# Kernel optimization log

Hardware: AMD Instinct MI355X
Metric: run time of the kernel (lower is better)

The kernel has to match this reference:

```python
import jax, jax.numpy as jnp
import numpy as np

N_NODES = 50000
N_EDGES = 800000
IN_C, HID_C, OUT_C = 256, 128, 64


def setup_inputs() -> dict:
    key = jax.random.key(0)
    k1, k2, k3, k4 = jax.random.split(key, 4)
    x = jax.random.normal(k1, (N_NODES, IN_C), dtype=jnp.float32)
    edge_index = jax.random.randint(k2, (2, N_EDGES), 0, N_NODES, dtype=jnp.int64)
    # Glorot-ish init for GCNConv weights; zero bias (PyG default)
    W1 = jax.random.normal(k3, (IN_C, HID_C), dtype=jnp.float32) * (1.0 / np.sqrt(IN_C))
    b1 = jnp.zeros((HID_C,), dtype=jnp.float32)
    W2 = jax.random.normal(k4, (HID_C, OUT_C), dtype=jnp.float32) * (1.0 / np.sqrt(HID_C))
    b2 = jnpform = jnp.zeros((OUT_C,), dtype=jnp.float32)
    return {"x": x, "edge_index": edge_index, "W1": W1, "b1": b1, "W2": W2, "b2": b2}


def _gcn_conv(x, src, dst, W, b, n_nodes):
    """PyG GCNConv: out = D^-1/2 (A+I) D^-1/2 x W + b (self-loops already in src/dst)."""
    h = x @ W  # [N, out] dense GEMM first (in >= out)
    deg = jax.ops.segment_sum(jnp.ones_like(dst, dtype=h.dtype), dst,
                              num_segments=n_nodes)  # includes self-loops -> deg >= 1
    dinv = jax.lax.rsqrt(jnp.maximum(deg, 1.0))
    norm = dinv[src] * dinv[dst]  # [E+N]
    msg = h[src] * norm[:, None]  # gather + scale
    out = jax.ops.segment_sum(msg, dst, num_segments=n_nodes)  # scatter-add
    return out + b


def reference(x, edge_index, W1, b1, W2, b2):
    n = x.shape[0]
    loops = jnp.arange(n, dtype=edge_index.dtype)
    src = jnp.concatenate([edge_index[0], loops])
    dst = jnp.concatenate([edge_index[1], loops])
    h = jax.nn.relu(_gcn_conv(x, src, dst, W1, b1, n))
    return _gcn_conv(h, src, dst, W2, b2, n)
```

## Files before the change

### kernel.cpp

```cpp
#include <hip/hip_runtime.h>

#define N_NODES 50000
#define N_EDGES 800000
#define IN_C    256
#define HID_C   128
#define OUT_C   64

#define SCAN_CHUNK 512
#define SCAN_NB ((N_NODES + SCAN_CHUNK - 1) / SCAN_CHUNK)

#define NBK 391
#define PCH 2048
#define NPB ((N_EDGES + PCH - 1) / PCH)

typedef __attribute__((ext_vector_type(8))) __bf16 bf16x8;
typedef __attribute__((ext_vector_type(4))) float f32x4;

__device__ __forceinline__ unsigned short f2bf(float f) {
    union { float f; unsigned int u; } c{f};
    unsigned int r = c.u + 0x7FFFu + ((c.u >> 16) & 1u);
    return (unsigned short)(r >> 16);
}
__device__ __forceinline__ float bf2f(unsigned short b) {
    union { unsigned int u; float f; } c{(unsigned int)b << 16};
    return c.f;
}

__global__ void deg_kernel(const int* __restrict__ src,
                           const int* __restrict__ dst,
                           unsigned int* __restrict__ deg, int E,
                           const float* __restrict__ W1,
                           const float* __restrict__ W2,
                           unsigned short* __restrict__ Wt1,
                           unsigned short* __restrict__ Wt2) {
    const int bid = blockIdx.x;
    const int t   = threadIdx.x;
    if (Wt1 != nullptr && bid < 40) {
        if (bid < 32) {
            int e = bid * 1024 + t * 4;
            float4 v = *(const float4*)&W1[e];
            int k = e >> 7, c = e & 127;
            Wt1[(c + 0) * IN_C + k] = f2bf(v.x);
            Wt1[(c + 1) * IN_C + k] = f2bf(v.y);
            Wt1[(c + 2) * IN_C + k] = f2bf(v.z);
            Wt1[(c + 3) * IN_C + k] = f2bf(v.w);
        } else {
            int e = (bid - 32) * 1024 + t * 4;
            float4 v = *(const float4*)&W2[e];
            int k = e >> 6, c = e & 63;
            Wt2[(c + 0) * HID_C + k] = f2bf(v.x);
            Wt2[(c + 1) * HID_C + k] = f2bf(v.y);
            Wt2[(c + 2) * HID_C + k] = f2bf(v.z);
            Wt2[(c + 3) * HID_C + k] = f2bf(v.w);
        }
    }
    int i = bid * blockDim.x + t;
    if (i < E) {
        int s = src[i];
        int d = dst[i];
        if ((unsigned)s < N_NODES && (unsigned)d < N_NODES)
            atomicAdd(&deg[d], 1u);
    }
}

__global__ __launch_bounds__(256) void scan1_kernel(
        unsigned int* __restrict__ cur, unsigned int* __restrict__ bsum,
        float* __restrict__ dinv, int N) {
    __shared__ unsigned int lds[256];
    const int b = blockIdx.x;
    const int t = threadIdx.x;
    const int i0 = b * SCAN_CHUNK + 2 * t;

    unsigned e0 = (i0     < N) ? cur[i0]     : 0u;
    unsigned e1 = (i0 + 1 < N) ? cur[i0 + 1] : 0u;
    if (i0     < N) dinv[i0]     = rsqrtf((float)(e0 + 1u));
    if (i0 + 1 < N) dinv[i0 + 1] = rsqrtf((float)(e1 + 1u));

    unsigned p = e0 + e1;
    lds[t] = p;
    __syncthreads();
    for (int off = 1; off < 256; off <<= 1) {
        unsigned v = (t >= off) ? lds[t - off] : 0u;
        __syncthreads();
        lds[t] += v;
        __syncthreads();
    }
    unsigned excl = lds[t] - p;
    if (t == 255) bsum[b] = lds[255];
    if (i0     < N) cur[i0]     = excl;
    if (i0 + 1 < N) cur[i0 + 1] = excl + e0;
}

__global__ __launch_bounds__(256) void scan2_kernel(
        unsigned int* __restrict__ cur, const unsigned int* __restrict__ bsum,
        int N) {
    __shared__ unsigned int lds[256];
    const int b = blockIdx.x;
    const int t = threadIdx.x;
    lds[t] = (t < b && t < SCAN_NB) ? bsum[t] : 0u;
    __syncthreads();
    for (int off = 128; off > 0; off >>= 1) {
        if (t < off) lds[t] += lds[t + off];
        __syncthreads();
    }
    const unsigned offset = lds[0];
    const int i0 = b * SCAN_CHUNK + 2 * t;
    if (i0     < N) cur[i0]     += offset;
    if (i0 + 1 < N) cur[i0 + 1] += offset;
}

__global__ void binit_kernel(const unsigned int* __restrict__ cur,
                             unsigned int* __restrict__ bcur,
                             unsigned int* __restrict__ bbase) {
    int t = threadIdx.x;
    if (t < NBK) {
        unsigned v = cur[t * 128];
        bcur[t]  = v;
        bbase[t] = v;
    }
    if (t == NBK) bbase[NBK] = N_EDGES;
}

template <int KDIM, int NDIM>
__global__ __launch_bounds__(256) void fused_gemm_part_kernel(
        const float* __restrict__ A, const unsigned short* __restrict__ Wt,
        const float* __restrict__ dinv,
        unsigned short* __restrict__ Cout, int M,
        const int* __restrict__ src, const int* __restrict__ dst,
        unsigned int* __restrict__ bcur,
        unsigned int* __restrict__ gpairs, int E) {
    __shared__ union {
        struct { unsigned short A[64][40]; unsigned short B[NDIM][40]; } g;
        struct { unsigned int pairs[PCH];
                 unsigned int counts[512];
                 unsigned int starts[513];
                 unsigned int gbase[NBK];
                 unsigned int temp[256]; } p;
    } sh;

    const int bid  = blockIdx.x;
    const int t    = threadIdx.x;
    const int role = bid % 3;
    const int pb   = bid / 3;

    if (role == 2) {
        const int base = pb * PCH;
        for (int i = t; i < 512; i += 256) sh.p.counts[i] = 0;
        __syncthreads();

        unsigned preg[PCH / 256], rreg[PCH / 256];
        bool val[PCH / 256];
#pragma unroll
        for (int j = 0; j < PCH / 256; ++j) {
            int i = base + j * 256 + t;
            val[j] = false;
            if (i < E) {
                int s = src[i], d = dst[i];
                if ((unsigned)s < N_NODES && (unsigned)d < N_NODES) {
                    val[j] = true;
                    unsigned bkt = (unsigned)d >> 7;
                    preg[j] = (bkt << 23) | (((unsigned)d & 127u) << 16) |
                              (unsigned)s;
                    rreg[j] = atomicAdd(&sh.p.counts[bkt], 1u);
                }
            }
        }
        __syncthreads();
        unsigned e0 = sh.p.counts[2 * t], e1 = sh.p.counts[2 * t + 1];
        unsigned pp = e0 + e1;
        sh.p.temp[t] = pp;
        __syncthreads();
        for (int off = 1; off < 256; off <<= 1) {
            unsigned v = (t >= off) ? sh.p.temp[t - off] : 0u;
            __syncthreads();
            sh.p.temp[t] += v;
            __syncthreads();
        }
        unsigned excl = sh.p.temp[t] - pp;
        sh.p.starts[2 * t]     = excl;
        sh.p.starts[2 * t + 1] = excl + e0;
        if (t == 255) sh.p.starts[512] = sh.p.temp[255];
        __syncthreads();
        for (int b = t; b < NBK; b += 256) {
            unsigned c = sh.p.counts[b];
            if (c) sh.p.gbase[b] = atomicAdd(&bcur[b], c);
        }
        __syncthreads();
#pragma unroll
        for (int j = 0; j < PCH / 256; ++j)
            if (val[j]) {
                unsigned bkt  = preg[j] >> 23;
                unsigned slot = sh.p.starts[bkt] + rreg[j];
                sh.p.pairs[slot] = preg[j];
            }
        __syncthreads();
        unsigned total = sh.p.starts[512];
        for (unsigned i = t; i < total; i += 256) {
            unsigned pd  = sh.p.pairs[i];
            unsigned bkt = pd >> 23;
            unsigned rank = i - sh.p.starts[bkt];
            gpairs[sh.p.gbase[bkt] + rank] = pd;
        }
        return;
    }

    const int gb = pb * 2 + role;
    if (gb >= (M + 63) / 64) return;
    constexpr int NF = NDIM / 16;
    const int block_row = gb * 64;
    const int w    = t >> 6;
    const int lane = t & 63;
    const int arow = lane & 15;
    const int g    = lane >> 4;

    f32x4 acc[NF] = {};

    for (int k0 = 0; k0 < KDIM; k0 += 32) {
#pragma unroll
        for (int q = 0; q < 2; ++q) {
            int u   = t * 2 + q;
            int row = u >> 3;
            int kq  = u & 7;
            int grow = block_row + row;
            if (grow >= M) grow = M - 1;
            float4 v = *(const float4*)&A[(size_t)grow * KDIM + k0 + kq * 4];
            ushort4 bb = {f2bf(v.x), f2bf(v.y), f2bf(v.z), f2bf(v.w)};
            *(ushort4*)&sh.g.A[row][kq * 4] = bb;
        }
        {
            constexpr int B8 = (NDIM * 4) / 256;
#pragma unroll
            for (int r = 0; r < B8; ++r) {
                int iu  = t * B8 + r;
                int col = iu >> 2;
                int k8  = iu & 3;
                *(uint4*)&sh.g.B[col][k8 * 8] =
                    *(const uint4*)&Wt[(size_t)col * KDIM + k0 + k8 * 8];
            }
        }
        __syncthreads();

        bf16x8 af = *(const bf16x8*)&sh.g.A[w * 16 + arow][g * 8];
#pragma unroll
        for (int f = 0; f < NF; ++f) {
            bf16x8 bf_ = *(const bf16x8*)&sh.g.B[f * 16 + arow][g * 8];
            acc[f] = __builtin_amdgcn_mfma_f32_16x16x32_bf16(af, bf_, acc[f],
                                                             0, 0, 0);
        }
        __syncthreads();
    }

#pragma unroll
    for (int i = 0; i < 4; ++i) {
        int row = block_row + w * 16 + g * 4 + i;
        if (row < M) {
            float dv = dinv[row];
#pragma unroll
            for (int f = 0; f < NF; ++f)
                Cout[(size_t)row * NDIM + f * 16 + arow] = f2bf(dv * acc[f][i]);
        }
    }
}

__global__ __launch_bounds__(256) void fine_fill_kernel(
        const unsigned int* __restrict__ gpairs,
        const unsigned int* __restrict__ bbase,
        unsigned int* __restrict__ cur,
        int* __restrict__ esrc, int N) {
    __shared__ unsigned int cnt[128];
    __shared__ unsigned int inc[128];
    const int b  = blockIdx.x;
    const int t  = threadIdx.x;
    const unsigned e0 = bbase[b], e1 = bbase[b + 1];
    const int node0 = b << 7;
    const int nn = min(128, N - node0);

    if (t < 128) cnt[t] = 0;
    __syncthreads();
    for (unsigned i = e0 + t; i < e1; i += 256) {
        unsigned dloc = (gpairs[i] >> 16) & 127u;
        atomicAdd(&cnt[dloc], 1u);
    }
    __syncthreads();
    if (t < 128) inc[t] = cnt[t];
    __syncthreads();
    for (int off = 1; off < 128; off <<= 1) {
        unsigned a = (t >= off && t < 128) ? inc[t - off] : 0u;
        __syncthreads();
        if (t < 128) inc[t] += a;
        __syncthreads();
    }
    if (t < 128) cnt[t] = inc[t] - cnt[t];
    __syncthreads();
    for (unsigned i = e0 + t; i < e1; i += 256) {
        unsigned pd   = gpairs[i];
        unsigned dloc = (pd >> 16) & 127u;
        unsigned r = atomicAdd(&cnt[dloc], 1u);
        esrc[e0 + r] = (int)(pd & 0xFFFFu);
    }
    __syncthreads();
    if (t < nn) cur[node0 + t] = e0 + inc[t];
}

template <int KDIM, int NDIM, bool ABF16>
__global__ __launch_bounds__(256) void mfma_gemm_kernel(
        const void* __restrict__ Ain, const unsigned short* __restrict__ Wt,
        const float* __restrict__ dinv,
        unsigned short* __restrict__ Cout, int M) {
    __shared__ unsigned short Alds[64][40];
    __shared__ unsigned short Blds[NDIM][40];

    const int t = threadIdx.x;
    constexpr int NF = NDIM / 16;
    const int block_row = blockIdx.x * 64;
    const int w    = t >> 6;
    const int lane = t & 63;
    const int arow = lane & 15;
    const int g    = lane >> 4;

    f32x4 acc[NF] = {};

    for (int k0 = 0; k0 < KDIM; k0 += 32) {
        if (ABF16) {
            const unsigned short* A = (const unsigned short*)Ain;
            int row = t >> 2;
            int k8  = t & 3;
            int grow = block_row + row;
            if (grow >= M) grow = M - 1;
            *(uint4*)&Alds[row][k8 * 8] =
                *(const uint4*)&A[(size_t)grow * KDIM + k0 + k8 * 8];
        } else {
            const float* A = (const float*)Ain;
#pragma unroll
            for (int q = 0; q < 2; ++q) {
                int u   = t * 2 + q;
                int row = u >> 3;
                int kq  = u & 7;
                int grow = block_row + row;
                if (grow >= M) grow = M - 1;
                float4 v = *(const float4*)&A[(size_t)grow * KDIM + k0 + kq * 4];
                ushort4 bb = {f2bf(v.x), f2bf(v.y), f2bf(v.z), f2bf(v.w)};
                *(ushort4*)&Alds[row][kq * 4] = bb;
            }
        }
        {
            constexpr int B8 = (NDIM * 4) / 256;
#pragma unroll
            for (int r = 0; r < B8; ++r) {
                int iu  = t * B8 + r;
                int col = iu >> 2;
                int k8  = iu & 3;
                *(uint4*)&Blds[col][k8 * 8] =
                    *(const uint4*)&Wt[(size_t)col * KDIM + k0 + k8 * 8];
            }
        }
        __syncthreads();

        bf16x8 af = *(const bf16x8*)&Alds[w * 16 + arow][g * 8];
#pragma unroll
        for (int f = 0; f < NF; ++f) {
            bf16x8 bf_ = *(const bf16x8*)&Blds[f * 16 + arow][g * 8];
            acc[f] = __builtin_amdgcn_mfma_f32_16x16x32_bf16(af, bf_, acc[f],
                                                             0, 0, 0);
        }
        __syncthreads();
    }

#pragma unroll
    for (int i = 0; i < 4; ++i) {
        int row = block_row + w * 16 + g * 4 + i;
        if (row < M) {
            float dv = dinv[row];
#pragma unroll
            for (int f = 0; f < NF; ++f)
                Cout[(size_t)row * NDIM + f * 16 + arow] = f2bf(dv * acc[f][i]);
        }
    }
}

template <int C, bool RELU, bool OUTBF16>
__global__ __launch_bounds__(256) void gather_kernel(
        const unsigned int* __restrict__ cur,
        const int* __restrict__ esrc,
        const float* __restrict__ dinv,
        const unsigned short* __restrict__ h,
        const float* __restrict__ bias,
        void* __restrict__ out, int N) {
    constexpr int G = C / 4;
    int tid  = blockIdx.x * blockDim.x + threadIdx.x;
    int v    = tid / G;
    int lane = tid % G;
    if (v >= N) return;
    unsigned int start = (v == 0) ? 0u : cur[v - 1];
    unsigned int end   = cur[v];

    ushort4 hs = *(const ushort4*)&h[(size_t)v * C + lane * 4];
    float4 a0 = {bf2f(hs.x), bf2f(hs.y), bf2f(hs.z), bf2f(hs.w)};
    float4 a1 = {0.f, 0.f, 0.f, 0.f};
    float4 a2 = {0.f, 0.f, 0.f, 0.f};
    float4 a3 = {0.f, 0.f, 0.f, 0.f};

    unsigned int e = start;
    for (; e + 4 <= end; e += 4) {
        int s0 = esrc[e + 0];
        int s1 = esrc[e + 1];
        int s2 = esrc[e + 2];
        int s3 = esrc[e + 3];
        ushort4 v0 = *(const ushort4*)&h[(size_t)s0 * C + lane * 4];
        ushort4 v1 = *(const ushort4*)&h[(size_t)s1 * C + lane * 4];
        ushort4 v2 = *(const ushort4*)&h[(size_t)s2 * C + lane * 4];
        ushort4 v3 = *(const ushort4*)&h[(size_t)s3 * C + lane * 4];
        a0.x += bf2f(v0.x); a0.y += bf2f(v0.y); a0.z += bf2f(v0.z); a0.w += bf2f(v0.w);
        a1.x += bf2f(v1.x); a1.y += bf2f(v1.y); a1.z += bf2f(v1.z); a1.w += bf2f(v1.w);
        a2.x += bf2f(v2.x); a2.y += bf2f(v2.y); a2.z += bf2f(v2.z); a2.w += bf2f(v2.w);
        a3.x += bf2f(v3.x); a3.y += bf2f(v3.y); a3.z += bf2f(v3.z); a3.w += bf2f(v3.w);
    }
    for (; e < end; ++e) {
        int s = esrc[e];
        ushort4 v0 = *(const ushort4*)&h[(size_t)s * C + lane * 4];
        a0.x += bf2f(v0.x); a0.y += bf2f(v0.y); a0.z += bf2f(v0.z); a0.w += bf2f(v0.w);
    }
    float4 acc;
    acc.x = (a0.x + a1.x) + (a2.x + a3.x);
    acc.y = (a0.y + a1.y) + (a2.y + a3.y);
    acc.z = (a0.z + a1.z) + (a2.z + a3.z);
    acc.w = (a0.w + a1.w) + (a2.w + a3.w);

    float dv = dinv[v];
    float4 b = *(const float4*)&bias[lane * 4];
    float4 r;
    r.x = fmaf(dv, acc.x, b.x);
    r.y = fmaf(dv, acc.y, b.y);
    r.z = fmaf(dv, acc.z, b.z);
    r.w = fmaf(dv, acc.w, b.w);
    if (RELU) {
        r.x = fmaxf(r.x, 0.f);
        r.y = fmaxf(r.y, 0.f);
        r.z = fmaxf(r.z, 0.f);
        r.w = fmaxf(r.w, 0.f);
    }
    if (OUTBF16) {
        ushort4 o = {f2bf(r.x), f2bf(r.y), f2bf(r.z), f2bf(r.w)};
        *(ushort4*)&((unsigned short*)out)[(size_t)v * C + lane * 4] = o;
    } else {
        *(float4*)&((float*)out)[(size_t)v * C + lane * 4] = r;
    }
}

template <int C, int C4>
__global__ void scatter_kernel(const int* __restrict__ src,
                               const int* __restrict__ dst,
                               const float* __restrict__ dinv,
                               const float* __restrict__ h,
                               float* __restrict__ out, int E) {
    int tid  = blockIdx.x * blockDim.x + threadIdx.x;
    int e    = tid / C4;
    int lane = tid % C4;
    if (e >= E) return;
    int s = src[e];
    int d = dst[e];
    if ((unsigned)s >= N_NODES || (unsigned)d >= N_NODES) return;
    float norm = dinv[s] * dinv[d];
    float4 v = *(const float4*)&h[(size_t)s * C + lane * 4];
    float* o = &out[(size_t)d * C + lane * 4];
    unsafeAtomicAdd(o + 0, v.x * norm);
    unsafeAtomicAdd(o + 1, v.y * norm);
    unsafeAtomicAdd(o + 2, v.z * norm);
    unsafeAtomicAdd(o + 3, v.w * norm);
}

__global__ void dinv_only_kernel(const unsigned int* __restrict__ deg,
                                 float* __restrict__ dinv, int N) {
    int i = blockIdx.x * blockDim.x + threadIdx.x;
    if (i < N) dinv[i] = rsqrtf((float)(deg[i] + 1u));
}

template <int BM, int BN, int BK, int TM, int TN, int KDIM, int NDIM>
__global__ __launch_bounds__(256) void gemm_kernel(
        const float* __restrict__ A, const float* __restrict__ B,
        float* __restrict__ Cout, int M) {
    __shared__ float As[BK][BM + 1];
    __shared__ float Bs[BK][BN];

    constexpr int TX = BN / TN;
    const int t  = threadIdx.x;
    const int tx = t % TX;
    const int ty = t / TX;
    const int block_row = blockIdx.x * BM;
    const int col_base  = blockIdx.y * BN;

    float acc[TM][TN] = {};

    for (int k0 = 0; k0 < KDIM; k0 += BK) {
        for (int i = t; i < BM * BK / 4; i += 256) {
            int row = i / (BK / 4);
            int c4  = i % (BK / 4);
            int grow = block_row + row;
            if (grow >= M) grow = M - 1;
            float4 v = *(const float4*)&A[(size_t)grow * KDIM + k0 + c4 * 4];
            As[c4 * 4 + 0][row] = v.x;
            As[c4 * 4 + 1][row] = v.y;
            As[c4 * 4 + 2][row] = v.z;
            As[c4 * 4 + 3][row] = v.w;
        }
        for (int i = t; i < BK * BN / 4; i += 256) {
            int row = i / (BN / 4);
            int c4  = i % (BN / 4);
            *(float4*)&Bs[row][c4 * 4] =
                *(const float4*)&B[(size_t)(k0 + row) * NDIM + col_base + c4 * 4];
        }
        __syncthreads();

#pragma unroll
        for (int kk = 0; kk < BK; ++kk) {
            float4 av = *(const float4*)&As[kk][ty * TM];
            float a_[4] = {av.x, av.y, av.z, av.w};
            float4 bv[TN / 4];
#pragma unroll
            for (int j4 = 0; j4 < TN / 4; ++j4)
                bv[j4] = *(const float4*)&Bs[kk][tx * 4 + j4 * (BN / 2)];
#pragma unroll
            for (int i = 0; i < TM; ++i) {
                float ai = a_[i];
#pragma unroll
                for (int j4 = 0; j4 < TN / 4; ++j4) {
                    acc[i][j4 * 4 + 0] = fmaf(ai, bv[j4].x, acc[i][j4 * 4 + 0]);
                    acc[i][j4 * 4 + 1] = fmaf(ai, bv[j4].y, acc[i][j4 * 4 + 1]);
                    acc[i][j4 * 4 + 2] = fmaf(ai, bv[j4].z, acc[i][j4 * 4 + 2]);
                    acc[i][j4 * 4 + 3] = fmaf(ai, bv[j4].w, acc[i][j4 * 4 + 3]);
                }
            }
        }
        __syncthreads();
    }

#pragma unroll
    for (int i = 0; i < TM; ++i) {
        int grow = block_row + ty * TM + i;
        if (grow < M) {
#pragma unroll
            for (int j4 = 0; j4 < TN / 4; ++j4) {
                float4 v = {acc[i][j4 * 4 + 0], acc[i][j4 * 4 + 1],
                            acc[i][j4 * 4 + 2], acc[i][j4 * 4 + 3]};
                *(float4*)&Cout[(size_t)grow * NDIM + col_base + tx * 4 +
                                j4 * (BN / 2)] = v;
            }
        }
    }
}

template <int C, bool RELU>
__global__ void epilogue_kernel(const float* __restrict__ agg,
                                const float* __restrict__ h,
                                const float* __restrict__ dinv,
                                const float* __restrict__ bias,
                                float* __restrict__ out, int N) {
    int tid = blockIdx.x * blockDim.x + threadIdx.x;
    int total = N * (C / 4);
    if (tid >= total) return;
    int c4  = tid % (C / 4);
    int row = tid / (C / 4);
    float d2 = dinv[row];
    d2 *= d2;
    float4 a  = *(const float4*)&agg[(size_t)tid * 4];
    float4 hv = *(const float4*)&h[(size_t)tid * 4];
    float4 b  = *(const float4*)&bias[c4 * 4];
    float4 r;
    r.x = a.x + hv.x * d2 + b.x;
    r.y = a.y + hv.y * d2 + b.y;
    r.z = a.z + hv.z * d2 + b.z;
    r.w = a.w + hv.w * d2 + b.w;
    if (RELU) {
        r.x = fmaxf(r.x, 0.f);
        r.y = fmaxf(r.y, 0.f);
        r.z = fmaxf(r.z, 0.f);
        r.w = fmaxf(r.w, 0.f);
    }
    *(float4*)&out[(size_t)tid * 4] = r;
}

extern "C" void kernel_launch(void* const* d_in, const int* in_sizes, int n_in,
                              void* d_out, int out_size, void* d_ws, size_t ws_size,
                              hipStream_t stream) {
    const float* x   = (const float*)d_in[0];
    const int*   ei  = (const int*)d_in[1];
    const float* W1  = (const float*)d_in[2];
    const float* b1  = (const float*)d_in[3];
    const float* W2  = (const float*)d_in[4];
    const float* b2  = (const float*)d_in[5];
    float*       out = (float*)d_out;

    const int* src = ei;
    const int* dst = ei + N_EDGES;

    char* ws = (char*)d_ws;
    size_t off = 0;
    auto alloc = [&](size_t bytes) {
        void* p = ws + off;
        off += (bytes + 255) & ~(size_t)255;
        return p;
    };

    unsigned int*   cur    = (unsigned int*)alloc(N_NODES * sizeof(unsigned int));
    unsigned int*   bsum   = (unsigned int*)alloc(SCAN_NB * sizeof(unsigned int));
    float*          dinv   = (float*)alloc(N_NODES * sizeof(float));
    int*            esrc   = (int*)alloc((size_t)N_EDGES * sizeof(int));
    unsigned int*   gpairs = (unsigned int*)alloc((size_t)N_EDGES * 4);
    unsigned int*   bbase  = (unsigned int*)alloc((NBK + 1) * sizeof(unsigned int));
    unsigned int*   bcur   = (unsigned int*)alloc(NBK * sizeof(unsigned int));
    unsigned short* Wt1    = (unsigned short*)alloc((size_t)IN_C * HID_C * 2);
    unsigned short* Wt2    = (unsigned short*)alloc((size_t)HID_C * OUT_C * 2);
    unsigned short* h1     = (unsigned short*)alloc((size_t)N_NODES * HID_C * 2);
    unsigned short* g1     = (unsigned short*)alloc((size_t)N_NODES * HID_C * 2);
    unsigned short* h2     = h1;
    size_t needed = off;

    if (ws_size >= needed) {
        hipMemsetAsync(cur, 0, N_NODES * sizeof(unsigned int), stream);

        deg_kernel<<<(N_EDGES + 255) / 256, 256, 0, stream>>>(
            src, dst, cur, N_EDGES, W1, W2, Wt1, Wt2);
        scan1_kernel<<<SCAN_NB, 256, 0, stream>>>(cur, bsum, dinv, N_NODES);
        scan2_kernel<<<SCAN_NB, 256, 0, stream>>>(cur, bsum, N_NODES);
        binit_kernel<<<1, 512, 0, stream>>>(cur, bcur, bbase);

        fused_gemm_part_kernel<IN_C, HID_C>
            <<<3 * NPB, 256, 0, stream>>>(x, Wt1, dinv, h1, N_NODES,
                                          src, dst, bcur, gpairs, N_EDGES);
        fine_fill_kernel<<<NBK, 256, 0, stream>>>(gpairs, bbase, cur, esrc,
                                                  N_NODES);
        {
            int total = N_NODES * (HID_C / 4);
            gather_kernel<HID_C, true, true>
                <<<(total + 255) / 256, 256, 0, stream>>>(cur, esrc, dinv, h1,
                                                          b1, g1, N_NODES);
        }
        mfma_gemm_kernel<HID_C, OUT_C, true>
            <<<(N_NODES + 63) / 64, 256, 0, stream>>>(g1, Wt2, dinv, h2,
                                                      N_NODES);
        {
            int total = N_NODES * (OUT_C / 4);
            gather_kernel<OUT_C, false, false>
                <<<(total + 255) / 256, 256, 0, stream>>>(cur, esrc, dinv, h2,
                                                          b2, out, N_NODES);
        }
    } else {
        off = 0;
        unsigned int* deg   = (unsigned int*)alloc(N_NODES * sizeof(unsigned int));
        float*        dinvF = (float*)alloc(N_NODES * sizeof(float));
        float*        h1F   = (float*)alloc((size_t)N_NODES * HID_C * sizeof(float));
        float*        agg1  = (float*)alloc((size_t)N_NODES * HID_C * sizeof(float));
        float*        h2F   = h1F;

        hipMemsetAsync(deg, 0, N_NODES * sizeof(unsigned int), stream);
        hipMemsetAsync(agg1, 0, (size_t)N_NODES * HID_C * sizeof(float), stream);
        hipMemsetAsync(out, 0, (size_t)N_NODES * OUT_C * sizeof(float), stream);

        deg_kernel<<<(N_EDGES + 255) / 256, 256, 0, stream>>>(
            src, dst, deg, N_EDGES, nullptr, nullptr, nullptr, nullptr);
        dinv_only_kernel<<<(N_NODES + 255) / 256, 256, 0, stream>>>(deg, dinvF,
                                                                    N_NODES);

        gemm_kernel<64, 64, 16, 4, 4, IN_C, HID_C>
            <<<dim3((N_NODES + 63) / 64, HID_C / 64), 256, 0, stream>>>(
                x, W1, h1F, N_NODES);
        {
            long long total = (long long)N_EDGES * (HID_C / 4);
            scatter_kernel<HID_C, HID_C / 4>
                <<<(unsigned)((total + 255) / 256), 256, 0, stream>>>(
                    src, dst, dinvF, h1F, agg1, N_EDGES);
        }
        {
            int total = N_NODES * (HID_C / 4);
            epilogue_kernel<HID_C, true>
                <<<(total + 255) / 256, 256, 0, stream>>>(agg1, h1F, dinvF, b1,
                                                          agg1, N_NODES);
        }
        gemm_kernel<64, 64, 16, 4, 4, HID_C, OUT_C>
            <<<dim3((N_NODES + 63) / 64, OUT_C / 64), 256, 0, stream>>>(
                agg1, W2, h2F, N_NODES);
        {
            long long total = (long long)N_EDGES * (OUT_C / 4);
            scatter_kernel<OUT_C, OUT_C / 4>
                <<<(unsigned)((total + 255) / 256), 256, 0, stream>>>(
                    src, dst, dinvF, h2F, out, N_EDGES);
        }
        {
            int total = N_NODES * (OUT_C / 4);
            epilogue_kernel<OUT_C, false>
                <<<(total + 255) / 256, 256, 0, stream>>>(out, h2F, dinvF, b2,
                                                          out, N_NODES);
        }
    }
}
```

Baseline: 149.3 us.

## Fuse layer-1 gather with layer-2 GEMM using per-block LDS weights

```diff
diff --git a/kernel.cpp b/kernel.cpp
--- a/kernel.cpp
+++ b/kernel.cpp
@@ -302,78 +302,110 @@
     if (t < nn) cur[node0 + t] = e0 + inc[t];
 }
 
-template <int KDIM, int NDIM, bool ABF16>
-__global__ __launch_bounds__(256) void mfma_gemm_kernel(
-        const void* __restrict__ Ain, const unsigned short* __restrict__ Wt,
+template <int CIN, int COUT>
+__global__ __launch_bounds__(256) void gather_gemm_kernel(
+        const unsigned int* __restrict__ cur,
+        const int* __restrict__ esrc,
         const float* __restrict__ dinv,
-        unsigned short* __restrict__ Cout, int M) {
-    __shared__ unsigned short Alds[64][40];
-    __shared__ unsigned short Blds[NDIM][40];
+        const unsigned short* __restrict__ h,
+        const float* __restrict__ bias1,
+        const unsigned short* __restrict__ Wt2,
+        unsigned short* __restrict__ h2, int N) {
+    constexpr int G    = CIN / 4;
+    constexpr int NPB8 = 256 / G;
+    constexpr int WSTR = CIN + 4;
+    __shared__ unsigned short W2lds[COUT][WSTR];
+    __shared__ float rows[NPB8][CIN];
 
     const int t = threadIdx.x;
-    constexpr int NF = NDIM / 16;
-    const int block_row = blockIdx.x * 64;
-    const int w    = t >> 6;
-    const int lane = t & 63;
-    const int arow = lane & 15;
-    const int g    = lane >> 4;
-
-    f32x4 acc[NF] = {};
-
-    for (int k0 = 0; k0 < KDIM; k0 += 32) {
-        if (ABF16) {
-            const unsigned short* A = (const unsigned short*)Ain;
-            int row = t >> 2;
-            int k8  = t & 3;
-            int grow = block_row + row;
-            if (grow >= M) grow = M - 1;
-            *(uint4*)&Alds[row][k8 * 8] =
-                *(const uint4*)&A[(size_t)grow * KDIM + k0 + k8 * 8];
-        } else {
-            const float* A = (const float*)Ain;
-#pragma unroll
-            for (int q = 0; q < 2; ++q) {
-                int u   = t * 2 + q;
-                int row = u >> 3;
-                int kq  = u & 7;
-                int grow = block_row + row;
-                if (grow >= M) grow = M - 1;
-                float4 v = *(const float4*)&A[(size_t)grow * KDIM + k0 + kq * 4];
-                ushort4 bb = {f2bf(v.x), f2bf(v.y), f2bf(v.z), f2bf(v.w)};
-                *(ushort4*)&Alds[row][kq * 4] = bb;
+    {
+        constexpr int UNITS = COUT * (CIN / 4);
+#pragma unroll
+        for (int r = 0; r < UNITS / 256; ++r) {
+            int u  = r * 256 + t;
+            int c  = u / (CIN / 4);
+            int kq = u % (CIN / 4);
+            *(uint2*)&W2lds[c][kq * 4] =
+                *(const uint2*)&Wt2[(size_t)c * CIN + kq * 4];
+        }
+    }
+
+    const int n    = t / G;
+    const int lane = t % G;
+    const int v    = blockIdx.x * NPB8 + n;
+    const bool valid = v < N;
+
+    if (valid) {
+        unsigned int start = (v == 0) ? 0u : cur[v - 1];
+        unsigned int end   = cur[v];
+
+        ushort4 hs = *(const ushort4*)&h[(size_t)v * CIN + lane * 4];
+        float4 a0 = {bf2f(hs.x), bf2f(hs.y), bf2f(hs.z), bf2f(hs.w)};
+        float4 a1 = {0.f, 0.f, 0.f, 0.f};
+        float4 a2 = {0.f, 0.f, 0.f, 0.f};
+        float4 a3 = {0.f, 0.f, 0.f, 0.f};
+
+        unsigned int e = start;
+        for (; e + 4 <= end; e += 4) {
+            int s0 = esrc[e + 0];
+            int s1 = esrc[e + 1];
+            int s2 = esrc[e + 2];
+            int s3 = esrc[e + 3];
+            ushort4 v0 = *(const ushort4*)&h[(size_t)s0 * CIN + lane * 4];
+            ushort4 v1 = *(const ushort4*)&h[(size_t)s1 * CIN + lane * 4];
+            ushort4 v2 = *(const ushort4*)&h[(size_t)s2 * CIN + lane * 4];
+            ushort4 v3 = *(const ushort4*)&h[(size_t)s3 * CIN + lane * 4];
+            a0.x += bf2f(v0.x); a0.y += bf2f(v0.y); a0.z += bf2f(v0.z); a0.w += bf2f(v0.w);
+            a1.x += bf2f(v1.x); a1.y += bf2f(v1.y); a1.z += bf2f(v1.z); a1.w += bf2f(v1.w);
+            a2.x += bf2f(v2.x); a2.y += bf2f(v2.y); a2.z += bf2f(v2.z); a2.w += bf2f(v2.w);
+            a3.x += bf2f(v3.x); a3.y += bf2f(v3.y); a3.z += bf2f(v3.z); a3.w += bf2f(v3.w);
+        }
+        for (; e < end; ++e) {
+            int s = esrc[e];
+            ushort4 v0 = *(const ushort4*)&h[(size_t)s * CIN + lane * 4];
+            a0.x += bf2f(v0.x); a0.y += bf2f(v0.y); a0.z += bf2f(v0.z); a0.w += bf2f(v0.w);
+        }
+        float4 acc;
+        acc.x = (a0.x + a1.x) + (a2.x + a3.x);
+        acc.y = (a0.y + a1.y) + (a2.y + a3.y);
+        acc.z = (a0.z + a1.z) + (a2.z + a3.z);
+        acc.w = (a0.w + a1.w) + (a2.w + a3.w);
+
+        float dv = dinv[v];
+        float4 b = *(const float4*)&bias1[lane * 4];
+        float4 r;
+        r.x = fmaxf(fmaf(dv, acc.x, b.x), 0.f);
+        r.y = fmaxf(fmaf(dv, acc.y, b.y), 0.f);
+        r.z = fmaxf(fmaf(dv, acc.z, b.z), 0.f);
+        r.w = fmaxf(fmaf(dv, acc.w, b.w), 0.f);
+        *(float4*)&rows[n][lane * 4] = r;
+    }
+    __syncthreads();
+
+    if (valid) {
+        float dv = dinv[v];
+#pragma unroll
+        for (int cc = 0; cc < COUT / G; ++cc) {
+            int c = lane + cc * G;
+            float acc = 0.f;
+#pragma unroll
+            for (int k = 0; k < CIN; k += 8) {
+                uint2 w0 = *(const uint2*)&W2lds[c][k];
+                uint2 w1 = *(const uint2*)&W2lds[c][k + 4];
+                float4 r0 = *(const float4*)&rows[n][k];
+                float4 r1 = *(const float4*)&rows[n][k + 4];
+                const unsigned short* wp0 = (const unsigned short*)&w0;
+                const unsigned short* wp1 = (const unsigned short*)&w1;
+                acc = fmaf(r0.x, bf2f(wp0[0]), acc);
+                acc = fmaf(r0.y, bf2f(wp0[1]), acc);
+                acc = fmaf(r0.z, bf2f(wp0[2]), acc);
+                acc = fmaf(r0.w, bf2f(wp0[3]), acc);
+                acc = fmaf(r1.x, bf2f(wp1[0]), acc);
+                acc = fmaf(r1.y, bf2f(wp1[1]), acc);
+                acc = fmaf(r1.z, bf2f(wp1[2]), acc);
+                acc = fmaf(r1.w, bf2f(wp1[3]), acc);
             }
-        }
-        {
-            constexpr int B8 = (NDIM * 4) / 256;
-#pragma unroll
-            for (int r = 0; r < B8; ++r) {
-                int iu  = t * B8 + r;
-                int col = iu >> 2;
-                int k8  = iu & 3;
-                *(uint4*)&Blds[col][k8 * 8] =
-                    *(const uint4*)&Wt[(size_t)col * KDIM + k0 + k8 * 8];
-            }
-        }
-        __syncthreads();
-
-        bf16x8 af = *(const bf16x8*)&Alds[w * 16 + arow][g * 8];
-#pragma unroll
-        for (int f = 0; f < NF; ++f) {
-            bf16x8 bf_ = *(const bf16x8*)&Blds[f * 16 + arow][g * 8];
-            acc[f] = __builtin_amdgcn_mfma_f32_16x16x32_bf16(af, bf_, acc[f],
-                                                             0, 0, 0);
-        }
-        __syncthreads();
-    }
-
-#pragma unroll
-    for (int i = 0; i < 4; ++i) {
-        int row = block_row + w * 16 + g * 4 + i;
-        if (row < M) {
-            float dv = dinv[row];
-#pragma unroll
-            for (int f = 0; f < NF; ++f)
-                Cout[(size_t)row * NDIM + f * 16 + arow] = f2bf(dv * acc[f][i]);
+            h2[(size_t)v * COUT + c] = f2bf(dv * acc);
         }
     }
 }
@@ -611,8 +643,7 @@
     unsigned short* Wt1    = (unsigned short*)alloc((size_t)IN_C * HID_C * 2);
     unsigned short* Wt2    = (unsigned short*)alloc((size_t)HID_C * OUT_C * 2);
     unsigned short* h1     = (unsigned short*)alloc((size_t)N_NODES * HID_C * 2);
-    unsigned short* g1     = (unsigned short*)alloc((size_t)N_NODES * HID_C * 2);
-    unsigned short* h2     = h1;
+    unsigned short* h2     = (unsigned short*)alloc((size_t)N_NODES * OUT_C * 2);
     size_t needed = off;
 
     if (ws_size >= needed) {
@@ -630,14 +661,11 @@
         fine_fill_kernel<<<NBK, 256, 0, stream>>>(gpairs, bbase, cur, esrc,
                                                   N_NODES);
         {
-            int total = N_NODES * (HID_C / 4);
-            gather_kernel<HID_C, true, true>
-                <<<(total + 255) / 256, 256, 0, stream>>>(cur, esrc, dinv, h1,
-                                                          b1, g1, N_NODES);
-        }
-        mfma_gemm_kernel<HID_C, OUT_C, true>
-            <<<(N_NODES + 63) / 64, 256, 0, stream>>>(g1, Wt2, dinv, h2,
-                                                      N_NODES);
+            int blocks = (N_NODES + 7) / 8;
+            gather_gemm_kernel<HID_C, OUT_C>
+                <<<blocks, 256, 0, stream>>>(cur, esrc, dinv, h1, b1, Wt2,
+                                             h2, N_NODES);
+        }
         {
             int total = N_NODES * (OUT_C / 4);
             gather_kernel<OUT_C, false, false>
```

Result: slower. 169.6 us (+13.6%).
